# Optimization experiments

Measured on AMD Instinct MI355X. Metric: run time of the kernel, lower is better.

## Reference

```python
import jax, jax.numpy as jnp
import numpy as np

LOCALITY = 10.0  # percentile for local masking (<=100 -> masking active)


def setup_inputs() -> dict:
    key = jax.random.key(0)
    k1, k2, k3, k4 = jax.random.split(key, 4)
    n_head, hid, v_dim = 8, 256, 32
    N, B = 4096, 2
    m_dist = jax.random.uniform(k1, (n_head, N, N), dtype=jnp.float32)
    x = jax.random.normal(k2, (B, N, hid), dtype=jnp.float32)
    r = jax.random.normal(k3, (n_head, 1, 1), dtype=jnp.float32)
    weight = jax.random.normal(k4, (n_head, hid, v_dim), dtype=jnp.float32) * (1.0 / np.sqrt(hid))
    return {"m_dist": m_dist, "x": x, "r": r, "weight": weight}


def reference(m_dist, x, r, weight):
    # per-head distance scale, derived from learned r
    scale = jnp.tan(0.25 * jnp.pi * (1 - 1e-07) * (1 + jnp.sin(r)))  # [h,1,1]
    scaled = m_dist * scale  # [h, Nq, Nk]
    # per-query percentile threshold -> local masking
    thr = jnp.percentile(scaled, LOCALITY, axis=-1, keepdims=True)  # [h, Nq, 1]
    scaled = jnp.where(scaled <= thr, scaled, jnp.inf)
    att = jax.nn.softmax(-scaled, axis=-1)  # [h, Nq, Nk]
    value = jnp.einsum('bnj,hjk->bhnk', x, weight)  # [b, h, Nk, v]
    out = jnp.einsum('hjn,bhnk->bhjk', att, value)  # [b, h, Nq, v]
    out = jnp.transpose(out, (0, 2, 1, 3))  # [b, Nq, h, v]
    b, nq = out.shape[0], out.shape[1]
    out = out.reshape(b, nq, -1)  # [b, Nq, hid]
    return jax.nn.gelu(out)
```

## Files before the change

### kernel.cpp

```cpp
#include <hip/hip_runtime.h>
#include <hip/hip_bf16.h>
#include <math.h>

#define NH   8
#define NSEQ 4096
#define NB   2
#define HID  256
#define VD   32
#define RANK 409
#define NBIN 128
#define CAND 704
#define TG   0.1171875f

typedef float floatx4 __attribute__((ext_vector_type(4)));

__device__ __forceinline__ unsigned mbcnt64(unsigned long long m) {
  return __builtin_amdgcn_mbcnt_hi((unsigned)(m >> 32),
                                   __builtin_amdgcn_mbcnt_lo((unsigned)m, 0u));
}
__device__ __forceinline__ float wred_min(float x) {
#pragma unroll
  for (int d = 32; d; d >>= 1) x = fminf(x, __shfl_xor(x, d, 64));
  return x;
}
__device__ __forceinline__ float wred_max(float x) {
#pragma unroll
  for (int d = 32; d; d >>= 1) x = fmaxf(x, __shfl_xor(x, d, 64));
  return x;
}
__device__ __forceinline__ float wred_sum(float x) {
#pragma unroll
  for (int d = 32; d; d >>= 1) x += __shfl_xor(x, d, 64);
  return x;
}
__device__ __forceinline__ float gelu_tanh(float x) {
  float x3 = x * x * x;
  float inner = 0.7978845608028654f * (x + 0.044715f * x3);
  return 0.5f * x * (1.0f + tanhf(inner));
}
__device__ __forceinline__ float bflo(unsigned u) { return __uint_as_float(u << 16); }
__device__ __forceinline__ float bfhi(unsigned u) { return __uint_as_float(u & 0xFFFF0000u); }


__global__ __launch_bounds__(256) void value_kernel(
    const float* __restrict__ x, const float* __restrict__ w,
    const float* __restrict__ r, __hip_bfloat16* __restrict__ value,
    float* __restrict__ scales) {
  const int tid = threadIdx.x;

  if (blockIdx.x == 0 && tid < NH) {
    double rv = (double)r[tid];
    const float c0 = (float)(0.25 * 3.141592653589793 * (1.0 - 1e-07));
    float s1 = (float)sin(rv);
    float t = c0 * (1.0f + s1);
    scales[tid] = (float)tan((double)t);
  }

  const int n0 = blockIdx.x * 8;
  __shared__ float sx[NB][8][HID];
#pragma unroll
  for (int i = 0; i < 16; i++) {
    int idx = i * 256 + tid;
    int b = idx >> 11;
    int rem = idx & 2047;
    int nn = rem >> 8;
    int j = rem & 255;
    sx[b][nn][j] = x[((size_t)b * NSEQ + n0 + nn) * HID + j];
  }
  __syncthreads();

  const int h = tid >> 5, k = tid & 31;
  float acc[NB][8];
#pragma unroll
  for (int b = 0; b < NB; b++)
#pragma unroll
    for (int nn = 0; nn < 8; nn++) acc[b][nn] = 0.f;

  const float* wp = w + (size_t)h * HID * VD + k;
  for (int j4 = 0; j4 < HID; j4 += 4) {
    float wv0 = wp[(size_t)(j4 + 0) * VD];
    float wv1 = wp[(size_t)(j4 + 1) * VD];
    float wv2 = wp[(size_t)(j4 + 2) * VD];
    float wv3 = wp[(size_t)(j4 + 3) * VD];
#pragma unroll
    for (int b = 0; b < NB; b++) {
#pragma unroll
      for (int nn = 0; nn < 8; nn++) {
        const float4 xv = *reinterpret_cast<const float4*>(&sx[b][nn][j4]);
        float a = acc[b][nn];
        a = fmaf(xv.x, wv0, a);
        a = fmaf(xv.y, wv1, a);
        a = fmaf(xv.z, wv2, a);
        a = fmaf(xv.w, wv3, a);
        acc[b][nn] = a;
      }
    }
  }
#pragma unroll
  for (int b = 0; b < NB; b++)
#pragma unroll
    for (int nn = 0; nn < 8; nn++)
      value[((size_t)h * NSEQ + n0 + nn) * (NB * VD) + b * VD + k] =
          __float2bfloat16(acc[b][nn]);
}


#define PROCR(CV, G, T)                                                            \
  do {                                                                             \
    const int nb_ = ((G) << 15) | (lane << 9);                                     \
    { bool s = (CV).x <= (T); unsigned long long m = __ballot(s);                  \
      unsigned p = nc + mbcnt64(m);                                                \
      if (s && p < CAND) sc[p] = make_float2((CV).x, __int_as_float(nb_));         \
      nc += (unsigned)__popcll(m); }                                               \
    { bool s = (CV).y <= (T); unsigned long long m = __ballot(s);                  \
      unsigned p = nc + mbcnt64(m);                                                \
      if (s && p < CAND) sc[p] = make_float2((CV).y, __int_as_float(nb_ | 128));   \
      nc += (unsigned)__popcll(m); }                                               \
    { bool s = (CV).z <= (T); unsigned long long m = __ballot(s);                  \
      unsigned p = nc + mbcnt64(m);                                                \
      if (s && p < CAND) sc[p] = make_float2((CV).z, __int_as_float(nb_ | 256));   \
      nc += (unsigned)__popcll(m); }                                               \
    { bool s = (CV).w <= (T); unsigned long long m = __ballot(s);                  \
      unsigned p = nc + mbcnt64(m);                                                \
      if (s && p < CAND) sc[p] = make_float2((CV).w, __int_as_float(nb_ | 384));   \
      nc += (unsigned)__popcll(m); }                                               \
  } while (0)

#define PROCS(CV, G, TS)                                                                  \
  do {                                                                                    \
    const int nb_ = ((G) << 15) | (lane << 9);                                            \
    { float t_ = (CV).x * scale; bool s = t_ <= (TS); unsigned long long m = __ballot(s); \
      unsigned p = nc + mbcnt64(m);                                                       \
      if (s && p < CAND) sc[p] = make_float2(t_, __int_as_float(nb_));                    \
      nc += (unsigned)__popcll(m); }                                                      \
    { float t_ = (CV).y * scale; bool s = t_ <= (TS); unsigned long long m = __ballot(s); \
      unsigned p = nc + mbcnt64(m);                                                       \
      if (s && p < CAND) sc[p] = make_float2(t_, __int_as_float(nb_ | 128));              \
      nc += (unsigned)__popcll(m); }                                                      \
    { float t_ = (CV).z * scale; bool s = t_ <= (TS); unsigned long long m = __ballot(s); \
      unsigned p = nc + mbcnt64(m);                                                       \
      if (s && p < CAND) sc[p] = make_float2(t_, __int_as_float(nb_ | 256));              \
      nc += (unsigned)__popcll(m); }                                                      \
    { float t_ = (CV).w * scale; bool s = t_ <= (TS); unsigned long long m = __ballot(s); \
      unsigned p = nc + mbcnt64(m);                                                       \
      if (s && p < CAND) sc[p] = make_float2(t_, __int_as_float(nb_ | 384));              \
      nc += (unsigned)__popcll(m); }                                                      \
  } while (0)

#define CNT1(U)                                                        \
  do {                                                                 \
    bool s_ = (U) <= Tc;                                               \
    cN += (unsigned)__popcll(__ballot(s_));                            \
    if (s_) vb = fmaxf(vb, (U)); else vs = fminf(vs, (U));             \
  } while (0)

__global__ __launch_bounds__(256, 6) void attn_kernel(
    const float* __restrict__ m_dist, const __hip_bfloat16* __restrict__ value,
    const float* __restrict__ scales, float* __restrict__ out) {
  const int tid = threadIdx.x;
  const int lane = tid & 63;
  const int wv = tid >> 6;
  const int bid = blockIdx.x;
  const int h = bid & 7;
  const int q = (bid >> 3) * 4 + wv;

  __shared__ float2 s_cand[4][CAND];
  __shared__ unsigned s_hist[4][NBIN];
  __shared__ float s_small[4][48];
  __shared__ unsigned s_cnt[4];

  float2* sc = s_cand[wv];
  unsigned* sh = s_hist[wv];
  float* ssm = s_small[wv];
  unsigned* scn = &s_cnt[wv];

  const float scale = scales[h];
  const floatx4* row4 =
      reinterpret_cast<const floatx4*>(m_dist + ((size_t)(h * NSEQ + q)) * NSEQ) + lane;

  unsigned nc = 0;
  {
    floatx4 c0 = __builtin_nontemporal_load(row4 + 0 * 64);
    floatx4 c1 = __builtin_nontemporal_load(row4 + 1 * 64);
    floatx4 n0 = __builtin_nontemporal_load(row4 + 2 * 64);
    floatx4 n1 = __builtin_nontemporal_load(row4 + 3 * 64);
    PROCR(c0, 0, TG); PROCR(c1, 1, TG);
    c0 = n0; c1 = n1;
    n0 = __builtin_nontemporal_load(row4 + 4 * 64);
    n1 = __builtin_nontemporal_load(row4 + 5 * 64);
    PROCR(c0, 2, TG); PROCR(c1, 3, TG);
    c0 = n0; c1 = n1;
    n0 = __builtin_nontemporal_load(row4 + 6 * 64);
    n1 = __builtin_nontemporal_load(row4 + 7 * 64);
    PROCR(c0, 4, TG); PROCR(c1, 5, TG);
    c0 = n0; c1 = n1;
    n0 = __builtin_nontemporal_load(row4 + 8 * 64);
    n1 = __builtin_nontemporal_load(row4 + 9 * 64);
    PROCR(c0, 6, TG); PROCR(c1, 7, TG);
    c0 = n0; c1 = n1;
    n0 = __builtin_nontemporal_load(row4 + 10 * 64);
    n1 = __builtin_nontemporal_load(row4 + 11 * 64);
    PROCR(c0, 8, TG); PROCR(c1, 9, TG);
    c0 = n0; c1 = n1;
    n0 = __builtin_nontemporal_load(row4 + 12 * 64);
    n1 = __builtin_nontemporal_load(row4 + 13 * 64);
    PROCR(c0, 10, TG); PROCR(c1, 11, TG);
    c0 = n0; c1 = n1;
    n0 = __builtin_nontemporal_load(row4 + 14 * 64);
    n1 = __builtin_nontemporal_load(row4 + 15 * 64);
    PROCR(c0, 12, TG); PROCR(c1, 13, TG);
    c0 = n0; c1 = n1;
    PROCR(c0, 14, TG); PROCR(c1, 15, TG);
  }

  float Tsel = TG;
  bool exact = false;
  float ex409 = 0.f, ex410 = 0.f;

  if (nc < (unsigned)(RANK + 2) || nc > (unsigned)CAND) {
    float lo, hi;
    if (nc < (unsigned)(RANK + 2)) { lo = TG; hi = 1.0f; }
    else { lo = 0.f; hi = TG; }
    bool collapse = false, ok = false;
    for (int it = 0; it < 40; ++it) {
      float mid = 0.5f * (lo + hi);
      if (!(mid > lo && mid < hi)) { collapse = true; break; }
      unsigned cN = 0;
      float vb = -INFINITY, vs = INFINITY;
      const float Tc = mid;
#pragma unroll 2
      for (int ch = 0; ch < 16; ++ch) {
        floatx4 cv = __builtin_nontemporal_load(row4 + ch * 64);
        CNT1(cv.x); CNT1(cv.y); CNT1(cv.z); CNT1(cv.w);
      }
      if (cN >= (unsigned)(RANK + 2) && cN <= (unsigned)CAND) { Tsel = mid; ok = true; break; }
      if (cN < (unsigned)(RANK + 2)) lo = mid; else hi = mid;
    }
    if (collapse) {
      unsigned cN = 0;
      float vb = -INFINITY, vs = INFINITY;
      {
        const float Tc = lo;
#pragma unroll 2
        for (int ch = 0; ch < 16; ++ch) {
          floatx4 cv = __builtin_nontemporal_load(row4 + ch * 64);
          CNT1(cv.x); CNT1(cv.y); CNT1(cv.z); CNT1(cv.w);
        }
      }
      vb = wred_max(vb);
      vs = wred_min(vs);
      float s409r, s410r;
      if (cN >= (unsigned)(RANK + 2)) { s409r = vb; s410r = vb; }
      else if (cN == (unsigned)(RANK + 1)) { s409r = vb; s410r = vs; }
      else { s409r = vs; s410r = vs; }
      ex409 = s409r * scale;
      ex410 = s410r * scale;
      exact = true;
      float thrS = 0.5f * ex409 + 0.5f * ex410;
      nc = 0;
#pragma unroll 2
      for (int ch = 0; ch < 16; ++ch) {
        floatx4 cv = __builtin_nontemporal_load(row4 + ch * 64);
        PROCS(cv, ch, thrS);
      }
    } else if (ok) {
      nc = 0;
      const float Tf = Tsel;
#pragma unroll 2
      for (int ch = 0; ch < 16; ++ch) {
        floatx4 cv = __builtin_nontemporal_load(row4 + ch * 64);
        PROCR(cv, ch, Tf);
      }
    }
  }
  if (nc > (unsigned)CAND) nc = (unsigned)CAND;
  const float smul = exact ? 1.0f : scale;

  sh[lane] = 0u;
  sh[lane + 64] = 0u;
  const float binscale = exact ? 0.f : (float)NBIN / Tsel;
  float mn = INFINITY;
  for (unsigned e = lane; e < nc; e += 64) {
    float vv = sc[e].x;
    mn = fminf(mn, vv);
    int b = (int)(vv * binscale);
    b = b < 0 ? 0 : (b > NBIN - 1 ? NBIN - 1 : b);
    atomicAdd(&sh[b], 1u);
  }
  const float minT = wred_min(mn) * smul;

  float v409, v410;
  if (exact) {
    v409 = ex409;
    v410 = ex410;
  } else {
    unsigned c2 = sh[2 * lane] + sh[2 * lane + 1];
    unsigned incl = c2;
#pragma unroll
    for (int d = 1; d < 64; d <<= 1) {
      unsigned o = __shfl_up(incl, d, 64);
      if (lane >= d) incl += o;
    }
    unsigned b2 = incl - c2;
    unsigned tb_l = 0, bt_l = 0;
    bool win = (b2 <= (unsigned)RANK && (unsigned)RANK < b2 + c2);
    if (win) {
      unsigned h0 = sh[2 * lane];
      if ((unsigned)RANK < b2 + h0) { tb_l = 2u * lane; bt_l = b2; }
      else { tb_l = 2u * lane + 1u; bt_l = b2 + h0; }
    }
    unsigned long long wm = __ballot(win);
    int wl = (int)__ffsll(wm) - 1;
    if (wl < 0) wl = 0;
    unsigned tb = (unsigned)__shfl((int)tb_l, wl, 64);
    unsigned base_tb = (unsigned)__shfl((int)bt_l, wl, 64);

    *scn = 0u;
    float mgt = INFINITY;
    for (unsigned e = lane; e < nc; e += 64) {
      float v = sc[e].x;
      int b = (int)(v * binscale);
      b = b < 0 ? 0 : (b > NBIN - 1 ? NBIN - 1 : b);
      if ((unsigned)b == tb) {
        unsigned p = atomicAdd(scn, 1u);
        if (p < 48u) ssm[p] = v;
      } else if ((unsigned)b > tb) {
        mgt = fminf(mgt, v);
      }
    }
    mgt = wred_min(mgt);
    unsigned cbin = *scn;

    float r409, r410;
    if (cbin <= 48u) {
      float cand = (lane < (int)cbin) ? ssm[lane] : INFINITY;
      unsigned less = 0, eq = 0;
      for (unsigned k = 0; k < cbin; k++) {
        float g = ssm[k];
        less += (g < cand) ? 1u : 0u;
        eq += (g == cand) ? 1u : 0u;
      }
      unsigned gl = base_tb + less;
      bool w9 = (lane < (int)cbin) && gl <= (unsigned)RANK && (unsigned)RANK < gl + eq;
      bool w10 = (lane < (int)cbin) && gl <= (unsigned)(RANK + 1) && (unsigned)(RANK + 1) < gl + eq;
      r409 = wred_min(w9 ? cand : INFINITY);
      float t10 = wred_min(w10 ? cand : INFINITY);
      r410 = isinf(t10) ? mgt : t10;
    } else {
      float a9 = INFINITY, a10 = INFINITY;
      for (unsigned e = lane; e < nc; e += 64) {
        float v = sc[e].x;
        int b = (int)(v * binscale);
        b = b < 0 ? 0 : (b > NBIN - 1 ? NBIN - 1 : b);
        if ((unsigned)b == tb) {
          unsigned less = 0, eq = 0;
          for (unsigned k = 0; k < nc; k++) {
            float g = sc[k].x;
            less += (g < v) ? 1u : 0u;
            eq += (g == v) ? 1u : 0u;
          }
          if (less <= (unsigned)RANK && (unsigned)RANK < less + eq) a9 = v;
          if (less <= (unsigned)(RANK + 1) && (unsigned)(RANK + 1) < less + eq) a10 = v;
        }
      }
      r409 = wred_min(a9);
      float t10 = wred_min(a10);
      r410 = isinf(t10) ? mgt : t10;
    }
    if (isinf(r409)) r409 = mgt;
    v409 = r409 * scale;
    v410 = r410 * scale;
  }
  const float thr = 0.5f * v409 + 0.5f * v410;

  float psum = 0.f;
  for (unsigned e = lane; e < nc; e += 64) {
    float2 t = sc[e];
    float ts = t.x * smul;
    float w = (ts <= thr) ? __expf(minT - ts) : 0.f;
    psum += w;
    sc[e] = make_float2(w, t.y);
  }
  const float denom = wred_sum(psum);
  const float invd = 1.0f / denom;
  const unsigned padded = (nc + 15u) & ~15u;
  if ((unsigned)lane < padded - nc) sc[nc + lane] = make_float2(0.f, __int_as_float(0));

  const int g = lane >> 3;
  const int c = lane & 7;
  const char* vpb = (const char*)value + (size_t)h * (NSEQ * 128) + c * 16;
  float a0 = 0.f, a1 = 0.f, a2 = 0.f, a3 = 0.f, a4 = 0.f, a5 = 0.f, a6 = 0.f, a7 = 0.f;
  for (unsigned t0 = 0; t0 < padded; t0 += 16) {
    float2 e0 = sc[t0 + g];
    float2 e1 = sc[t0 + 8 + g];
    const uint4 u0 = *reinterpret_cast<const uint4*>(vpb + __float_as_int(e0.y));
    const uint4 u1 = *reinterpret_cast<const uint4*>(vpb + __float_as_int(e1.y));
    float w0 = e0.x, w1 = e1.x;
    a0 = fmaf(w0, bflo(u0.x), a0);
    a1 = fmaf(w0, bfhi(u0.x), a1);
    a2 = fmaf(w0, bflo(u0.y), a2);
    a3 = fmaf(w0, bfhi(u0.y), a3);
    a4 = fmaf(w0, bflo(u0.z), a4);
    a5 = fmaf(w0, bfhi(u0.z), a5);
    a6 = fmaf(w0, bflo(u0.w), a6);
    a7 = fmaf(w0, bfhi(u0.w), a7);
    a0 = fmaf(w1, bflo(u1.x), a0);
    a1 = fmaf(w1, bfhi(u1.x), a1);
    a2 = fmaf(w1, bflo(u1.y), a2);
    a3 = fmaf(w1, bfhi(u1.y), a3);
    a4 = fmaf(w1, bflo(u1.z), a4);
    a5 = fmaf(w1, bfhi(u1.z), a5);
    a6 = fmaf(w1, bflo(u1.w), a6);
    a7 = fmaf(w1, bfhi(u1.w), a7);
  }
#pragma unroll
  for (int d = 8; d < 64; d <<= 1) {
    a0 += __shfl_xor(a0, d, 64);
    a1 += __shfl_xor(a1, d, 64);
    a2 += __shfl_xor(a2, d, 64);
    a3 += __shfl_xor(a3, d, 64);
    a4 += __shfl_xor(a4, d, 64);
    a5 += __shfl_xor(a5, d, 64);
    a6 += __shfl_xor(a6, d, 64);
    a7 += __shfl_xor(a7, d, 64);
  }

  if (lane < 8) {
    int col = c * 8;
    int bb = col >> 5, kk = col & 31;
    float* op = &out[((size_t)bb * NSEQ + q) * (NH * VD) + (size_t)h * VD + kk];
    float4 lo4 = make_float4(gelu_tanh(a0 * invd), gelu_tanh(a1 * invd),
                             gelu_tanh(a2 * invd), gelu_tanh(a3 * invd));
    float4 hi4 = make_float4(gelu_tanh(a4 * invd), gelu_tanh(a5 * invd),
                             gelu_tanh(a6 * invd), gelu_tanh(a7 * invd));
    *reinterpret_cast<float4*>(op) = lo4;
    *reinterpret_cast<float4*>(op + 4) = hi4;
  }
}


extern "C" void kernel_launch(void* const* d_in, const int* in_sizes, int n_in,
                              void* d_out, int out_size, void* d_ws, size_t ws_size,
                              hipStream_t stream) {
  const float* m_dist = (const float*)d_in[0];
  const float* x = (const float*)d_in[1];
  const float* r = (const float*)d_in[2];
  const float* w = (const float*)d_in[3];
  float* out = (float*)d_out;

  __hip_bfloat16* value = (__hip_bfloat16*)d_ws;
  float* scales = (float*)((char*)d_ws + (8u << 20));

  value_kernel<<<dim3(NSEQ / 8), dim3(256), 0, stream>>>(x, w, r, value, scales);
  attn_kernel<<<dim3(NH * NSEQ / 4), dim3(256), 0, stream>>>(m_dist, value, scales, out);
}
```

Measured before the change: 202.2 us.

## Process two query rows per wavefront and compact selected candidates before gather

Each wavefront now handles two query rows, with their row loads interleaved to raise memory-level parallelism. The block shrinks to 128 threads with launch bounds (128,3). The weighting pass now keeps only candidates under the threshold, so the value gather skips zero-weight entries. The gather loop is widened to four entries per step per row, interleaving the two rows' independent loads. The cost is higher register pressure and lower occupancy, and doing the selection logic twice serially could add per-wave latency.

```diff
diff --git a/kernel.cpp b/kernel.cpp
--- a/kernel.cpp
+++ b/kernel.cpp
@@ -104,6 +104,27 @@
           __float2bfloat16(acc[b][nn]);
 }
 
+
+#define PROCD(CV, G, SC, NC)                                                       \
+  do {                                                                             \
+    const int nb_ = ((G) << 15) | (lane << 9);                                     \
+    { bool s = (CV).x <= TG; unsigned long long m = __ballot(s);                   \
+      unsigned p = NC + mbcnt64(m);                                                \
+      if (s && p < CAND) SC[p] = make_float2((CV).x, __int_as_float(nb_));         \
+      NC += (unsigned)__popcll(m); }                                               \
+    { bool s = (CV).y <= TG; unsigned long long m = __ballot(s);                   \
+      unsigned p = NC + mbcnt64(m);                                                \
+      if (s && p < CAND) SC[p] = make_float2((CV).y, __int_as_float(nb_ | 128));   \
+      NC += (unsigned)__popcll(m); }                                               \
+    { bool s = (CV).z <= TG; unsigned long long m = __ballot(s);                   \
+      unsigned p = NC + mbcnt64(m);                                                \
+      if (s && p < CAND) SC[p] = make_float2((CV).z, __int_as_float(nb_ | 256));   \
+      NC += (unsigned)__popcll(m); }                                               \
+    { bool s = (CV).w <= TG; unsigned long long m = __ballot(s);                   \
+      unsigned p = NC + mbcnt64(m);                                                \
+      if (s && p < CAND) SC[p] = make_float2((CV).w, __int_as_float(nb_ | 384));   \
+      NC += (unsigned)__popcll(m); }                                               \
+  } while (0)
 
 #define PROCR(CV, G, T)                                                            \
   do {                                                                             \
@@ -154,65 +175,10 @@
     if (s_) vb = fmaxf(vb, (U)); else vs = fminf(vs, (U));             \
   } while (0)
 
-__global__ __launch_bounds__(256, 6) void attn_kernel(
-    const float* __restrict__ m_dist, const __hip_bfloat16* __restrict__ value,
-    const float* __restrict__ scales, float* __restrict__ out) {
-  const int tid = threadIdx.x;
-  const int lane = tid & 63;
-  const int wv = tid >> 6;
-  const int bid = blockIdx.x;
-  const int h = bid & 7;
-  const int q = (bid >> 3) * 4 + wv;
-
-  __shared__ float2 s_cand[4][CAND];
-  __shared__ unsigned s_hist[4][NBIN];
-  __shared__ float s_small[4][48];
-  __shared__ unsigned s_cnt[4];
-
-  float2* sc = s_cand[wv];
-  unsigned* sh = s_hist[wv];
-  float* ssm = s_small[wv];
-  unsigned* scn = &s_cnt[wv];
-
-  const float scale = scales[h];
-  const floatx4* row4 =
-      reinterpret_cast<const floatx4*>(m_dist + ((size_t)(h * NSEQ + q)) * NSEQ) + lane;
-
-  unsigned nc = 0;
-  {
-    floatx4 c0 = __builtin_nontemporal_load(row4 + 0 * 64);
-    floatx4 c1 = __builtin_nontemporal_load(row4 + 1 * 64);
-    floatx4 n0 = __builtin_nontemporal_load(row4 + 2 * 64);
-    floatx4 n1 = __builtin_nontemporal_load(row4 + 3 * 64);
-    PROCR(c0, 0, TG); PROCR(c1, 1, TG);
-    c0 = n0; c1 = n1;
-    n0 = __builtin_nontemporal_load(row4 + 4 * 64);
-    n1 = __builtin_nontemporal_load(row4 + 5 * 64);
-    PROCR(c0, 2, TG); PROCR(c1, 3, TG);
-    c0 = n0; c1 = n1;
-    n0 = __builtin_nontemporal_load(row4 + 6 * 64);
-    n1 = __builtin_nontemporal_load(row4 + 7 * 64);
-    PROCR(c0, 4, TG); PROCR(c1, 5, TG);
-    c0 = n0; c1 = n1;
-    n0 = __builtin_nontemporal_load(row4 + 8 * 64);
-    n1 = __builtin_nontemporal_load(row4 + 9 * 64);
-    PROCR(c0, 6, TG); PROCR(c1, 7, TG);
-    c0 = n0; c1 = n1;
-    n0 = __builtin_nontemporal_load(row4 + 10 * 64);
-    n1 = __builtin_nontemporal_load(row4 + 11 * 64);
-    PROCR(c0, 8, TG); PROCR(c1, 9, TG);
-    c0 = n0; c1 = n1;
-    n0 = __builtin_nontemporal_load(row4 + 12 * 64);
-    n1 = __builtin_nontemporal_load(row4 + 13 * 64);
-    PROCR(c0, 10, TG); PROCR(c1, 11, TG);
-    c0 = n0; c1 = n1;
-    n0 = __builtin_nontemporal_load(row4 + 14 * 64);
-    n1 = __builtin_nontemporal_load(row4 + 15 * 64);
-    PROCR(c0, 12, TG); PROCR(c1, 13, TG);
-    c0 = n0; c1 = n1;
-    PROCR(c0, 14, TG); PROCR(c1, 15, TG);
-  }
-
+__device__ __forceinline__ void sel_weight(
+    const floatx4* row4, const float scale, float2* sc, unsigned nc,
+    unsigned* sh, float* ssm, unsigned* scn, const int lane,
+    float& invd_out, unsigned& padded_out) {
   float Tsel = TG;
   bool exact = false;
   float ex409 = 0.f, ex410 = 0.f;
@@ -374,67 +340,197 @@
   const float thr = 0.5f * v409 + 0.5f * v410;
 
   float psum = 0.f;
+  unsigned mq = 0;
   for (unsigned e = lane; e < nc; e += 64) {
     float2 t = sc[e];
     float ts = t.x * smul;
-    float w = (ts <= thr) ? __expf(minT - ts) : 0.f;
+    bool sel = (ts <= thr);
+    float w = sel ? __expf(minT - ts) : 0.f;
     psum += w;
-    sc[e] = make_float2(w, t.y);
-  }
+    unsigned long long m = __ballot(sel);
+    unsigned p = mq + mbcnt64(m);
+    if (sel) sc[p] = make_float2(w, t.y);
+    mq += (unsigned)__popcll(m);
+  }
+  mq = (unsigned)__shfl((int)mq, 0, 64);
   const float denom = wred_sum(psum);
-  const float invd = 1.0f / denom;
-  const unsigned padded = (nc + 15u) & ~15u;
-  if ((unsigned)lane < padded - nc) sc[nc + lane] = make_float2(0.f, __int_as_float(0));
+  invd_out = 1.0f / denom;
+  const unsigned padded = (mq + 31u) & ~31u;
+  for (unsigned e = mq + lane; e < padded; e += 64) sc[e] = make_float2(0.f, __int_as_float(0));
+  padded_out = padded;
+}
+
+#define GATHER4(SEG, T0, A0, A1, A2, A3, A4, A5, A6, A7)                       \
+  do {                                                                         \
+    float2 e0 = SEG[(T0) + g];                                                 \
+    float2 e1 = SEG[(T0) + 8 + g];                                             \
+    float2 e2 = SEG[(T0) + 16 + g];                                            \
+    float2 e3 = SEG[(T0) + 24 + g];                                            \
+    const uint4 u0 = *reinterpret_cast<const uint4*>(vpb + __float_as_int(e0.y)); \
+    const uint4 u1 = *reinterpret_cast<const uint4*>(vpb + __float_as_int(e1.y)); \
+    const uint4 u2 = *reinterpret_cast<const uint4*>(vpb + __float_as_int(e2.y)); \
+    const uint4 u3 = *reinterpret_cast<const uint4*>(vpb + __float_as_int(e3.y)); \
+    float w0 = e0.x, w1 = e1.x, w2 = e2.x, w3 = e3.x;                          \
+    A0 = fmaf(w0, bflo(u0.x), A0); A1 = fmaf(w0, bfhi(u0.x), A1);              \
+    A2 = fmaf(w0, bflo(u0.y), A2); A3 = fmaf(w0, bfhi(u0.y), A3);              \
+    A4 = fmaf(w0, bflo(u0.z), A4); A5 = fmaf(w0, bfhi(u0.z), A5);              \
+    A6 = fmaf(w0, bflo(u0.w), A6); A7 = fmaf(w0, bfhi(u0.w), A7);              \
+    A0 = fmaf(w1, bflo(u1.x), A0); A1 = fmaf(w1, bfhi(u1.x), A1);              \
+    A2 = fmaf(w1, bflo(u1.y), A2); A3 = fmaf(w1, bfhi(u1.y), A3);              \
+    A4 = fmaf(w1, bflo(u1.z), A4); A5 = fmaf(w1, bfhi(u1.z), A5);              \
+    A6 = fmaf(w1, bflo(u1.w), A6); A7 = fmaf(w1, bfhi(u1.w), A7);              \
+    A0 = fmaf(w2, bflo(u2.x), A0); A1 = fmaf(w2, bfhi(u2.x), A1);              \
+    A2 = fmaf(w2, bflo(u2.y), A2); A3 = fmaf(w2, bfhi(u2.y), A3);              \
+    A4 = fmaf(w2, bflo(u2.z), A4); A5 = fmaf(w2, bfhi(u2.z), A5);              \
+    A6 = fmaf(w2, bflo(u2.w), A6); A7 = fmaf(w2, bfhi(u2.w), A7);              \
+    A0 = fmaf(w3, bflo(u3.x), A0); A1 = fmaf(w3, bfhi(u3.x), A1);              \
+    A2 = fmaf(w3, bflo(u3.y), A2); A3 = fmaf(w3, bfhi(u3.y), A3);              \
+    A4 = fmaf(w3, bflo(u3.z), A4); A5 = fmaf(w3, bfhi(u3.z), A5);              \
+    A6 = fmaf(w3, bflo(u3.w), A6); A7 = fmaf(w3, bfhi(u3.w), A7);              \
+  } while (0)
+
+__global__ __launch_bounds__(128, 3) void attn_kernel(
+    const float* __restrict__ m_dist, const __hip_bfloat16* __restrict__ value,
+    const float* __restrict__ scales, float* __restrict__ out) {
+  const int tid = threadIdx.x;
+  const int lane = tid & 63;
+  const int wv = tid >> 6;
+  const int bid = blockIdx.x;
+  const int h = bid & 7;
+  const int qA = (bid >> 3) * 4 + wv * 2;
+  const int qB = qA + 1;
+
+  __shared__ float2 s_cand[2][2][CAND];
+  __shared__ unsigned s_hist[2][2][NBIN];
+  __shared__ float s_small[2][2][48];
+  __shared__ unsigned s_cnt[2][2];
+
+  float2* scA = s_cand[wv][0];
+  float2* scB = s_cand[wv][1];
+
+  const float scale = scales[h];
+  const floatx4* rowA =
+      reinterpret_cast<const floatx4*>(m_dist + ((size_t)(h * NSEQ + qA)) * NSEQ) + lane;
+  const floatx4* rowB =
+      reinterpret_cast<const floatx4*>(m_dist + ((size_t)(h * NSEQ + qB)) * NSEQ) + lane;
+
+  unsigned ncA = 0, ncB = 0;
+  {
+    floatx4 aC0 = __builtin_nontemporal_load(rowA + 0 * 64);
+    floatx4 aC1 = __builtin_nontemporal_load(rowA + 1 * 64);
+    floatx4 bC0 = __builtin_nontemporal_load(rowB + 0 * 64);
+    floatx4 bC1 = __builtin_nontemporal_load(rowB + 1 * 64);
+    floatx4 aN0 = __builtin_nontemporal_load(rowA + 2 * 64);
+    floatx4 aN1 = __builtin_nontemporal_load(rowA + 3 * 64);
+    floatx4 bN0 = __builtin_nontemporal_load(rowB + 2 * 64);
+    floatx4 bN1 = __builtin_nontemporal_load(rowB + 3 * 64);
+    PROCD(aC0, 0, scA, ncA); PROCD(bC0, 0, scB, ncB);
+    PROCD(aC1, 1, scA, ncA); PROCD(bC1, 1, scB, ncB);
+    aC0 = aN0; aC1 = aN1; bC0 = bN0; bC1 = bN1;
+    aN0 = __builtin_nontemporal_load(rowA + 4 * 64);
+    aN1 = __builtin_nontemporal_load(rowA + 5 * 64);
+    bN0 = __builtin_nontemporal_load(rowB + 4 * 64);
+    bN1 = __builtin_nontemporal_load(rowB + 5 * 64);
+    PROCD(aC0, 2, scA, ncA); PROCD(bC0, 2, scB, ncB);
+    PROCD(aC1, 3, scA, ncA); PROCD(bC1, 3, scB, ncB);
+    aC0 = aN0; aC1 = aN1; bC0 = bN0; bC1 = bN1;
+    aN0 = __builtin_nontemporal_load(rowA + 6 * 64);
+    aN1 = __builtin_nontemporal_load(rowA + 7 * 64);
+    bN0 = __builtin_nontemporal_load(rowB + 6 * 64);
+    bN1 = __builtin_nontemporal_load(rowB + 7 * 64);
+    PROCD(aC0, 4, scA, ncA); PROCD(bC0, 4, scB, ncB);
+    PROCD(aC1, 5, scA, ncA); PROCD(bC1, 5, scB, ncB);
+    aC0 = aN0; aC1 = aN1; bC0 = bN0; bC1 = bN1;
+    aN0 = __builtin_nontemporal_load(rowA + 8 * 64);
+    aN1 = __builtin_nontemporal_load(rowA + 9 * 64);
+    bN0 = __builtin_nontemporal_load(rowB + 8 * 64);
+    bN1 = __builtin_nontemporal_load(rowB + 9 * 64);
+    PROCD(aC0, 6, scA, ncA); PROCD(bC0, 6, scB, ncB);
+    PROCD(aC1, 7, scA, ncA); PROCD(bC1, 7, scB, ncB);
+    aC0 = aN0; aC1 = aN1; bC0 = bN0; bC1 = bN1;
+    aN0 = __builtin_nontemporal_load(rowA + 10 * 64);
+    aN1 = __builtin_nontemporal_load(rowA + 11 * 64);
+    bN0 = __builtin_nontemporal_load(rowB + 10 * 64);
+    bN1 = __builtin_nontemporal_load(rowB + 11 * 64);
+    PROCD(aC0, 8, scA, ncA); PROCD(bC0, 8, scB, ncB);
+    PROCD(aC1, 9, scA, ncA); PROCD(bC1, 9, scB, ncB);
+    aC0 = aN0; aC1 = aN1; bC0 = bN0; bC1 = bN1;
+    aN0 = __builtin_nontemporal_load(rowA + 12 * 64);
+    aN1 = __builtin_nontemporal_load(rowA + 13 * 64);
+    bN0 = __builtin_nontemporal_load(rowB + 12 * 64);
+    bN1 = __builtin_nontemporal_load(rowB + 13 * 64);
+    PROCD(aC0, 10, scA, ncA); PROCD(bC0, 10, scB, ncB);
+    PROCD(aC1, 11, scA, ncA); PROCD(bC1, 11, scB, ncB);
+    aC0 = aN0; aC1 = aN1; bC0 = bN0; bC1 = bN1;
+    aN0 = __builtin_nontemporal_load(rowA + 14 * 64);
+    aN1 = __builtin_nontemporal_load(rowA + 15 * 64);
+    bN0 = __builtin_nontemporal_load(rowB + 14 * 64);
+    bN1 = __builtin_nontemporal_load(rowB + 15 * 64);
+    PROCD(aC0, 12, scA, ncA); PROCD(bC0, 12, scB, ncB);
+    PROCD(aC1, 13, scA, ncA); PROCD(bC1, 13, scB, ncB);
+    aC0 = aN0; aC1 = aN1; bC0 = bN0; bC1 = bN1;
+    PROCD(aC0, 14, scA, ncA); PROCD(bC0, 14, scB, ncB);
+    PROCD(aC1, 15, scA, ncA); PROCD(bC1, 15, scB, ncB);
+  }
+
+  float invdA, invdB;
+  unsigned padA, padB;
+  sel_weight(rowA, scale, scA, ncA, s_hist[wv][0], s_small[wv][0], &s_cnt[wv][0],
+             lane, invdA, padA);
+  sel_weight(rowB, scale, scB, ncB, s_hist[wv][1], s_small[wv][1], &s_cnt[wv][1],
+             lane, invdB, padB);
 
   const int g = lane >> 3;
   const int c = lane & 7;
   const char* vpb = (const char*)value + (size_t)h * (NSEQ * 128) + c * 16;
-  float a0 = 0.f, a1 = 0.f, a2 = 0.f, a3 = 0.f, a4 = 0.f, a5 = 0.f, a6 = 0.f, a7 = 0.f;
-  for (unsigned t0 = 0; t0 < padded; t0 += 16) {
-    float2 e0 = sc[t0 + g];
-    float2 e1 = sc[t0 + 8 + g];
-    const uint4 u0 = *reinterpret_cast<const uint4*>(vpb + __float_as_int(e0.y));
-    const uint4 u1 = *reinterpret_cast<const uint4*>(vpb + __float_as_int(e1.y));
-    float w0 = e0.x, w1 = e1.x;
-    a0 = fmaf(w0, bflo(u0.x), a0);
-    a1 = fmaf(w0, bfhi(u0.x), a1);
-    a2 = fmaf(w0, bflo(u0.y), a2);
-    a3 = fmaf(w0, bfhi(u0.y), a3);
-    a4 = fmaf(w0, bflo(u0.z), a4);
-    a5 = fmaf(w0, bfhi(u0.z), a5);
-    a6 = fmaf(w0, bflo(u0.w), a6);
-    a7 = fmaf(w0, bfhi(u0.w), a7);
-    a0 = fmaf(w1, bflo(u1.x), a0);
-    a1 = fmaf(w1, bfhi(u1.x), a1);
-    a2 = fmaf(w1, bflo(u1.y), a2);
-    a3 = fmaf(w1, bfhi(u1.y), a3);
-    a4 = fmaf(w1, bflo(u1.z), a4);
-    a5 = fmaf(w1, bfhi(u1.z), a5);
-    a6 = fmaf(w1, bflo(u1.w), a6);
-    a7 = fmaf(w1, bfhi(u1.w), a7);
+  float x0 = 0.f, x1 = 0.f, x2 = 0.f, x3 = 0.f, x4 = 0.f, x5 = 0.f, x6 = 0.f, x7 = 0.f;
+  float y0 = 0.f, y1 = 0.f, y2 = 0.f, y3 = 0.f, y4 = 0.f, y5 = 0.f, y6 = 0.f, y7 = 0.f;
+  const unsigned tmax = padA > padB ? padA : padB;
+  for (unsigned t0 = 0; t0 < tmax; t0 += 32) {
+    if (t0 < padA) GATHER4(scA, t0, x0, x1, x2, x3, x4, x5, x6, x7);
+    if (t0 < padB) GATHER4(scB, t0, y0, y1, y2, y3, y4, y5, y6, y7);
   }
 #pragma unroll
   for (int d = 8; d < 64; d <<= 1) {
-    a0 += __shfl_xor(a0, d, 64);
-    a1 += __shfl_xor(a1, d, 64);
-    a2 += __shfl_xor(a2, d, 64);
-    a3 += __shfl_xor(a3, d, 64);
-    a4 += __shfl_xor(a4, d, 64);
-    a5 += __shfl_xor(a5, d, 64);
-    a6 += __shfl_xor(a6, d, 64);
-    a7 += __shfl_xor(a7, d, 64);
+    x0 += __shfl_xor(x0, d, 64);
+    x1 += __shfl_xor(x1, d, 64);
+    x2 += __shfl_xor(x2, d, 64);
+    x3 += __shfl_xor(x3, d, 64);
+    x4 += __shfl_xor(x4, d, 64);
+    x5 += __shfl_xor(x5, d, 64);
+    x6 += __shfl_xor(x6, d, 64);
+    x7 += __shfl_xor(x7, d, 64);
+    y0 += __shfl_xor(y0, d, 64);
+    y1 += __shfl_xor(y1, d, 64);
+    y2 += __shfl_xor(y2, d, 64);
+    y3 += __shfl_xor(y3, d, 64);
+    y4 += __shfl_xor(y4, d, 64);
+    y5 += __shfl_xor(y5, d, 64);
+    y6 += __shfl_xor(y6, d, 64);
+    y7 += __shfl_xor(y7, d, 64);
   }
 
   if (lane < 8) {
     int col = c * 8;
     int bb = col >> 5, kk = col & 31;
-    float* op = &out[((size_t)bb * NSEQ + q) * (NH * VD) + (size_t)h * VD + kk];
-    float4 lo4 = make_float4(gelu_tanh(a0 * invd), gelu_tanh(a1 * invd),
-                             gelu_tanh(a2 * invd), gelu_tanh(a3 * invd));
-    float4 hi4 = make_float4(gelu_tanh(a4 * invd), gelu_tanh(a5 * invd),
-                             gelu_tanh(a6 * invd), gelu_tanh(a7 * invd));
-    *reinterpret_cast<float4*>(op) = lo4;
-    *reinterpret_cast<float4*>(op + 4) = hi4;
+    {
+      float* op = &out[((size_t)bb * NSEQ + qA) * (NH * VD) + (size_t)h * VD + kk];
+      float4 lo4 = make_float4(gelu_tanh(x0 * invdA), gelu_tanh(x1 * invdA),
+                               gelu_tanh(x2 * invdA), gelu_tanh(x3 * invdA));
+      float4 hi4 = make_float4(gelu_tanh(x4 * invdA), gelu_tanh(x5 * invdA),
+                               gelu_tanh(x6 * invdA), gelu_tanh(x7 * invdA));
+      *reinterpret_cast<float4*>(op) = lo4;
+      *reinterpret_cast<float4*>(op + 4) = hi4;
+    }
+    {
+      float* op = &out[((size_t)bb * NSEQ + qB) * (NH * VD) + (size_t)h * VD + kk];
+      float4 lo4 = make_float4(gelu_tanh(y0 * invdB), gelu_tanh(y1 * invdB),
+                               gelu_tanh(y2 * invdB), gelu_tanh(y3 * invdB));
+      float4 hi4 = make_float4(gelu_tanh(y4 * invdB), gelu_tanh(y5 * invdB),
+                               gelu_tanh(y6 * invdB), gelu_tanh(y7 * invdB));
+      *reinterpret_cast<float4*>(op) = lo4;
+      *reinterpret_cast<float4*>(op + 4) = hi4;
+    }
   }
 }
 
@@ -452,5 +548,5 @@
   float* scales = (float*)((char*)d_ws + (8u << 20));
 
   value_kernel<<<dim3(NSEQ / 8), dim3(256), 0, stream>>>(x, w, r, value, scales);
-  attn_kernel<<<dim3(NH * NSEQ / 4), dim3(256), 0, stream>>>(m_dist, value, scales, out);
-}
+  attn_kernel<<<dim3(NH * NSEQ / 4), dim3(128), 0, stream>>>(m_dist, value, scales, out);
+}
```

Result: slower. 224.1 us (+10.8%).
